# Kernel optimization log

Measured on AMD Instinct MI355X. Metric: run time of the kernel, lower is better.

The kernel has to match this reference:

```python
import jax, jax.numpy as jnp
import numpy as np
import math

B, S, C = 4, 8, 1024
DK = 1024
MAX_LEN = 8192
TOKEN_IND = 4095


def setup_inputs() -> dict:
    key = jax.random.key(0)
    k1, k2, k3, k4 = jax.random.split(key, 4)
    x = jax.random.normal(k1, (B, S, C), dtype=jnp.float32)
    W = jax.random.normal(k2, (C, 3 * DK), dtype=jnp.float32) * (1.0 / math.sqrt(C))
    b = jnp.zeros((3 * DK,), dtype=jnp.float32)
    key_cache = jax.random.normal(k3, (B, MAX_LEN, DK), dtype=jnp.float32)
    value_cache = jax.random.normal(k4, (B, MAX_LEN, DK), dtype=jnp.float32)
    return {"x": x, "W": W, "b": b, "key_cache": key_cache,
            "value_cache": value_cache, "token_ind": TOKEN_IND}


def reference(x, W, b, key_cache, value_cache, token_ind):
    # decode step: only the last token of x is used
    x_last = x[:, -1:, :]                        # [B, 1, C]
    qkv = x_last @ W + b                         # [B, 1, 3*dk]
    q, k_new, v_new = jnp.split(qkv, 3, axis=-1)  # each [B, 1, dk]
    dk = q.shape[-1]

    # scatter new k/v into cache at token_ind, then slice valid prefix
    key_cache = key_cache.at[:, token_ind:token_ind + 1, :].set(k_new)
    value_cache = value_cache.at[:, token_ind:token_ind + 1, :].set(v_new)
    size = token_ind + 1
    k = key_cache[:, :size, :]                   # [B, size, dk]
    v = value_cache[:, :size, :]                 # [B, size, dk]

    # scores for the single query against the whole valid cache
    weights = jnp.einsum('btc,bTc->btT', q, k) / math.sqrt(dk)  # [B, 1, size]

    # faithful broadcast quirk of the original: tril mask (size,size)
    # broadcasts weights [B,1,size] up to [B,size,size]
    mask = jnp.tril(jnp.ones((size, size), dtype=weights.dtype))
    logits = jnp.where(mask == 0, jnp.asarray(-9e15, weights.dtype), weights)  # [B, size, size]
    attention = jax.nn.softmax(logits, axis=-1)
    values = jnp.einsum('btT,bTc->btc', attention, v)  # [B, size, dk]
    return values
```

## Files before the change

kernel.cpp:

```cpp
#include <hip/hip_runtime.h>
#include <stdint.h>

#define B_      4
#define S_      8
#define C_      1024
#define DK_     1024
#define MAXLEN_ 8192
#define SIZE_   4096
#define NCH     64
#define CHR     64
#define NTOK    (SIZE_ - 1)

typedef unsigned short ushort_t;
typedef unsigned int   uint_t;
typedef float f32x4 __attribute__((ext_vector_type(4)));

__device__ __forceinline__ float bf2f(ushort_t u) {
    union { uint_t u; float f; } v; v.u = ((uint_t)u) << 16; return v.f;
}
__device__ __forceinline__ ushort_t f2bf(float f) {
    union { float f; uint_t u; } v; v.f = f;
    uint_t u = v.u;
    uint_t lsb = (u >> 16) & 1u;
    u += 0x7fffu + lsb;
    return (ushort_t)(u >> 16);
}

__global__ void __launch_bounds__(256) k_qkv_partial(
        const float* __restrict__ x, const float* __restrict__ W,
        float* __restrict__ part) {
    __shared__ float xs[B_][128];
    __shared__ float red[8][32][16];
    int t  = threadIdx.x;
    int cg_ = t & 31;
    int rg  = t >> 5;
    int c0 = blockIdx.x * 128;
    int r0 = blockIdx.y * 128;

    for (int i = t; i < B_ * 128; i += 256) {
        int b = i >> 7, r = i & 127;
        xs[b][r] = x[((b * S_) + (S_ - 1)) * C_ + r0 + r];
    }
    __syncthreads();

    float acc[B_][4] = {};
    const float* wp = W + (size_t)(r0 + rg * 16) * (3 * DK_) + c0 + cg_ * 4;
#pragma unroll 8
    for (int i = 0; i < 16; ++i) {
        f32x4 wv = *(const f32x4*)(wp + (size_t)i * (3 * DK_));
        int r = rg * 16 + i;
#pragma unroll
        for (int b = 0; b < B_; ++b) {
            float xv = xs[b][r];
            acc[b][0] += xv * wv[0];
            acc[b][1] += xv * wv[1];
            acc[b][2] += xv * wv[2];
            acc[b][3] += xv * wv[3];
        }
    }
#pragma unroll
    for (int b = 0; b < B_; ++b)
#pragma unroll
        for (int cc = 0; cc < 4; ++cc)
            red[rg][cg_][b * 4 + cc] = acc[b][cc];
    __syncthreads();

    if (t < 32) {
#pragma unroll
        for (int b = 0; b < B_; ++b) {
            float s0 = 0.f, s1 = 0.f, s2 = 0.f, s3 = 0.f;
#pragma unroll
            for (int r = 0; r < 8; ++r) {
                s0 += red[r][t][b * 4 + 0];
                s1 += red[r][t][b * 4 + 1];
                s2 += red[r][t][b * 4 + 2];
                s3 += red[r][t][b * 4 + 3];
            }
            f32x4 v = { s0, s1, s2, s3 };
            *(f32x4*)(part + (size_t)blockIdx.y * (B_ * 3 * DK_) + b * (3 * DK_) + c0 + t * 4) = v;
        }
    }
}

__global__ void __launch_bounds__(256) k_qkv_finish(
        const float* __restrict__ part, const float* __restrict__ bias,
        float* __restrict__ qkvws) {
    int i   = blockIdx.x * 256 + threadIdx.x;
    int bq  = i / 3072;
    int col = i - bq * 3072;
    float s = bias[col];
#pragma unroll
    for (int rt = 0; rt < 8; ++rt) s += part[rt * (B_ * 3 * DK_) + i];
    qkvws[(col >> 10) * (B_ * DK_) + bq * DK_ + (col & (DK_ - 1))] = s;
}

__global__ void __launch_bounds__(1024) k_scores_sum(
        const float* __restrict__ kc, const float* __restrict__ vc,
        const float* __restrict__ qkvws, ushort_t* __restrict__ es_bf,
        float* __restrict__ Ec, ushort_t* __restrict__ Pc) {
    __shared__ float es_l[CHR];
    __shared__ float ec_l[16];
    __shared__ f32x4 sub[4][256];
    int t    = threadIdx.x;
    int c    = blockIdx.x;
    int b    = blockIdx.y;
    int lane = t & 63;
    int wv   = t >> 6;
    int rg   = t >> 8;
    int tc   = t & 255;
    int d0   = tc * 4;

    {
        const float* qp = qkvws + b * DK_ + lane * 4;
        f32x4 q0 = *(const f32x4*)(qp);
        f32x4 q1 = *(const f32x4*)(qp + 256);
        f32x4 q2 = *(const f32x4*)(qp + 512);
        f32x4 q3 = *(const f32x4*)(qp + 768);
        int j0 = c * CHR + wv * 4;
        float esum = 0.f;
#pragma unroll
        for (int r = 0; r < 4; ++r) {
            int j = j0 + r;
            const float* kp = (j == NTOK)
                ? (qkvws + (B_ * DK_) + b * DK_)
                : (kc + ((size_t)b * MAXLEN_ + j) * DK_);
            kp += lane * 4;
            f32x4 k0 = *(const f32x4*)(kp);
            f32x4 k1 = *(const f32x4*)(kp + 256);
            f32x4 k2 = *(const f32x4*)(kp + 512);
            f32x4 k3 = *(const f32x4*)(kp + 768);
            float acc = k0[0]*q0[0] + k0[1]*q0[1] + k0[2]*q0[2] + k0[3]*q0[3]
                      + k1[0]*q1[0] + k1[1]*q1[1] + k1[2]*q1[2] + k1[3]*q1[3]
                      + k2[0]*q2[0] + k2[1]*q2[1] + k2[2]*q2[2] + k2[3]*q2[3]
                      + k3[0]*q3[0] + k3[1]*q3[1] + k3[2]*q3[2] + k3[3]*q3[3];
#pragma unroll
            for (int off = 32; off > 0; off >>= 1) acc += __shfl_down(acc, off, 64);
            if (lane == 0) {
                float e = __expf(acc * 0.03125f);
                es_l[wv * 4 + r] = e;
                es_bf[b * SIZE_ + j] = f2bf(e);
                esum += e;
            }
        }
        if (lane == 0) ec_l[wv] = esum;
    }
    __syncthreads();
    if (t == 0) {
        float s = 0.f;
#pragma unroll
        for (int i = 0; i < 16; ++i) s += ec_l[i];
        Ec[b * NCH + c] = s;
    }

    {
        const float* vbase = vc + ((size_t)b * MAXLEN_ + c * CHR + rg * 16) * DK_ + d0;
        bool subst = (c == NCH - 1) && (rg == 3);
        f32x4 a = { 0.f, 0.f, 0.f, 0.f };
#pragma unroll
        for (int i = 0; i < 16; ++i) {
            const float* vp = (subst && i == 15)
                ? (qkvws + 2 * (B_ * DK_) + b * DK_ + d0)
                : (vbase + (size_t)i * DK_);
            f32x4 u = *(const f32x4*)(vp);
            a += es_l[rg * 16 + i] * u;
        }
        sub[rg][tc] = a;
        __syncthreads();
        if (rg == 0) {
            f32x4 tot = a + sub[1][tc] + sub[2][tc] + sub[3][tc];
            ushort4 pv;
            pv.x = f2bf(tot[0]); pv.y = f2bf(tot[1]);
            pv.z = f2bf(tot[2]); pv.w = f2bf(tot[3]);
            *(ushort4*)(Pc + ((size_t)(b * NCH + c)) * DK_ + d0) = pv;
        }
    }
}

__global__ void __launch_bounds__(1024) k_out(
        const float* __restrict__ vc, const float* __restrict__ qkvws,
        const ushort_t* __restrict__ es_bf, const float* __restrict__ Ec,
        const ushort_t* __restrict__ Pc, float* __restrict__ out) {
    __shared__ float es_l[CHR];
    __shared__ float invS[CHR];
    __shared__ f32x4 sub[4][256];
    __shared__ f32x4 pre[4][256];
    int t  = threadIdx.x;
    int c  = blockIdx.x;
    int b  = blockIdx.y;
    int rg = t >> 8;
    int tc = t & 255;
    int d0 = tc * 4;

    if (t < 64) {
        float e = bf2f(es_bf[b * SIZE_ + c * CHR + t]);
        es_l[t] = e;
        float p = (t < c) ? Ec[b * NCH + t] : 0.f;
#pragma unroll
        for (int off = 32; off > 0; off >>= 1) p += __shfl_down(p, off, 64);
        float E0 = __shfl(p, 0, 64);
        float sc = e;
#pragma unroll
        for (int off = 1; off < 64; off <<= 1) {
            float o = __shfl_up(sc, off, 64);
            if (t >= off) sc += o;
        }
        invS[t] = 1.0f / (E0 + sc);
    }

    f32x4 vrow[16];
    {
        const float* vbase = vc + ((size_t)b * MAXLEN_ + c * CHR + rg * 16) * DK_ + d0;
        bool subst = (c == NCH - 1) && (rg == 3);
#pragma unroll
        for (int i = 0; i < 16; ++i) {
            const float* vp = (subst && i == 15)
                ? (qkvws + 2 * (B_ * DK_) + b * DK_ + d0)
                : (vbase + (size_t)i * DK_);
            vrow[i] = *(const f32x4*)(vp);
        }
    }

    {
        f32x4 p = { 0.f, 0.f, 0.f, 0.f };
        const ushort_t* pp = Pc + (size_t)b * NCH * DK_ + d0;
        for (int cc = rg; cc < c; cc += 4) {
            ushort4 pv = *(const ushort4*)(pp + (size_t)cc * DK_);
            p[0] += bf2f(pv.x); p[1] += bf2f(pv.y);
            p[2] += bf2f(pv.z); p[3] += bf2f(pv.w);
        }
        pre[rg][tc] = p;
    }
    __syncthreads();

    f32x4 a = { 0.f, 0.f, 0.f, 0.f };
#pragma unroll
    for (int i = 0; i < 16; ++i) a += es_l[rg * 16 + i] * vrow[i];
    sub[rg][tc] = a;
    __syncthreads();

    f32x4 acc = pre[0][tc] + pre[1][tc] + pre[2][tc] + pre[3][tc];
#pragma unroll
    for (int g = 0; g < 3; ++g)
        if (g < rg) acc += sub[g][tc];

    float* obase = out + ((size_t)b * SIZE_ + c * CHR + rg * 16) * DK_ + d0;
#pragma unroll
    for (int i = 0; i < 16; ++i) {
        acc += es_l[rg * 16 + i] * vrow[i];
        float is = invS[rg * 16 + i];
        f32x4 ov = { acc[0] * is, acc[1] * is, acc[2] * is, acc[3] * is };
        __builtin_nontemporal_store(ov, (f32x4*)(obase + (size_t)i * DK_));
    }
}

extern "C" void kernel_launch(void* const* d_in, const int* in_sizes, int n_in,
                              void* d_out, int out_size, void* d_ws, size_t ws_size,
                              hipStream_t stream) {
    (void)in_sizes; (void)n_in; (void)out_size; (void)ws_size;
    const float* x    = (const float*)d_in[0];
    const float* W    = (const float*)d_in[1];
    const float* bias = (const float*)d_in[2];
    const float* kc   = (const float*)d_in[3];
    const float* vc   = (const float*)d_in[4];
    float* out        = (float*)d_out;

    float* ws       = (float*)d_ws;
    float* part     = ws;
    float* qkvws    = ws + 131072;
    ushort_t* es_bf = (ushort_t*)(ws + 143360);
    float* Ec       = ws + 151552;
    ushort_t* Pc    = (ushort_t*)ws;

    hipLaunchKernelGGL(k_qkv_partial, dim3(24, 8), dim3(256),  0, stream, x, W, part);
    hipLaunchKernelGGL(k_qkv_finish,  dim3(48),    dim3(256),  0, stream, part, bias, qkvws);
    hipLaunchKernelGGL(k_scores_sum,  dim3(64, 4), dim3(1024), 0, stream, kc, vc, qkvws, es_bf, Ec, Pc);
    hipLaunchKernelGGL(k_out,         dim3(64, 4), dim3(1024), 0, stream, vc, qkvws, es_bf, Ec, Pc, out);
}
```

Before: 294.6 us.

## Fuse scores and output kernels with decoupled-lookback chunk prefix via flags

Merges the score/partial-sum kernel and the output kernel into one kernel. Each block publishes its chunk's fp32 partial V-sum and exp-sum, then spin-waits on per-chunk flags for all earlier chunks before building its prefix. This avoids a second launch, re-reading the V rows and the bf16 round-trips for the intermediate exps and partials. The cost is a dependence on all 256 blocks being co-resident, since a block stalled behind unscheduled earlier chunks could deadlock, plus spin-wait overhead and fp32 traffic for the published partials.

```diff
diff --git a/kernel.cpp b/kernel.cpp
--- a/kernel.cpp
+++ b/kernel.cpp
@@ -11,20 +11,8 @@
 #define CHR     64
 #define NTOK    (SIZE_ - 1)
 
-typedef unsigned short ushort_t;
-typedef unsigned int   uint_t;
+typedef unsigned int uint_t;
 typedef float f32x4 __attribute__((ext_vector_type(4)));
-
-__device__ __forceinline__ float bf2f(ushort_t u) {
-    union { uint_t u; float f; } v; v.u = ((uint_t)u) << 16; return v.f;
-}
-__device__ __forceinline__ ushort_t f2bf(float f) {
-    union { float f; uint_t u; } v; v.f = f;
-    uint_t u = v.u;
-    uint_t lsb = (u >> 16) & 1u;
-    u += 0x7fffu + lsb;
-    return (ushort_t)(u >> 16);
-}
 
 __global__ void __launch_bounds__(256) k_qkv_partial(
         const float* __restrict__ x, const float* __restrict__ W,
@@ -84,7 +72,8 @@
 
 __global__ void __launch_bounds__(256) k_qkv_finish(
         const float* __restrict__ part, const float* __restrict__ bias,
-        float* __restrict__ qkvws) {
+        float* __restrict__ qkvws, uint_t* __restrict__ flags) {
+    if (blockIdx.x == 0) flags[threadIdx.x] = 0;
     int i   = blockIdx.x * 256 + threadIdx.x;
     int bq  = i / 3072;
     int col = i - bq * 3072;
@@ -94,13 +83,16 @@
     qkvws[(col >> 10) * (B_ * DK_) + bq * DK_ + (col & (DK_ - 1))] = s;
 }
 
-__global__ void __launch_bounds__(1024) k_scores_sum(
+__global__ void __launch_bounds__(1024) k_attn(
         const float* __restrict__ kc, const float* __restrict__ vc,
-        const float* __restrict__ qkvws, ushort_t* __restrict__ es_bf,
-        float* __restrict__ Ec, ushort_t* __restrict__ Pc) {
+        const float* __restrict__ qkvws, float* __restrict__ PcPub,
+        float* __restrict__ EcPub, uint_t* __restrict__ flags,
+        float* __restrict__ out) {
     __shared__ float es_l[CHR];
     __shared__ float ec_l[16];
+    __shared__ float invS[CHR];
     __shared__ f32x4 sub[4][256];
+    __shared__ f32x4 pre[4][256];
     int t    = threadIdx.x;
     int c    = blockIdx.x;
     int b    = blockIdx.y;
@@ -138,74 +130,12 @@
             if (lane == 0) {
                 float e = __expf(acc * 0.03125f);
                 es_l[wv * 4 + r] = e;
-                es_bf[b * SIZE_ + j] = f2bf(e);
                 esum += e;
             }
         }
         if (lane == 0) ec_l[wv] = esum;
     }
     __syncthreads();
-    if (t == 0) {
-        float s = 0.f;
-#pragma unroll
-        for (int i = 0; i < 16; ++i) s += ec_l[i];
-        Ec[b * NCH + c] = s;
-    }
-
-    {
-        const float* vbase = vc + ((size_t)b * MAXLEN_ + c * CHR + rg * 16) * DK_ + d0;
-        bool subst = (c == NCH - 1) && (rg == 3);
-        f32x4 a = { 0.f, 0.f, 0.f, 0.f };
-#pragma unroll
-        for (int i = 0; i < 16; ++i) {
-            const float* vp = (subst && i == 15)
-                ? (qkvws + 2 * (B_ * DK_) + b * DK_ + d0)
-                : (vbase + (size_t)i * DK_);
-            f32x4 u = *(const f32x4*)(vp);
-            a += es_l[rg * 16 + i] * u;
-        }
-        sub[rg][tc] = a;
-        __syncthreads();
-        if (rg == 0) {
-            f32x4 tot = a + sub[1][tc] + sub[2][tc] + sub[3][tc];
-            ushort4 pv;
-            pv.x = f2bf(tot[0]); pv.y = f2bf(tot[1]);
-            pv.z = f2bf(tot[2]); pv.w = f2bf(tot[3]);
-            *(ushort4*)(Pc + ((size_t)(b * NCH + c)) * DK_ + d0) = pv;
-        }
-    }
-}
-
-__global__ void __launch_bounds__(1024) k_out(
-        const float* __restrict__ vc, const float* __restrict__ qkvws,
-        const ushort_t* __restrict__ es_bf, const float* __restrict__ Ec,
-        const ushort_t* __restrict__ Pc, float* __restrict__ out) {
-    __shared__ float es_l[CHR];
-    __shared__ float invS[CHR];
-    __shared__ f32x4 sub[4][256];
-    __shared__ f32x4 pre[4][256];
-    int t  = threadIdx.x;
-    int c  = blockIdx.x;
-    int b  = blockIdx.y;
-    int rg = t >> 8;
-    int tc = t & 255;
-    int d0 = tc * 4;
-
-    if (t < 64) {
-        float e = bf2f(es_bf[b * SIZE_ + c * CHR + t]);
-        es_l[t] = e;
-        float p = (t < c) ? Ec[b * NCH + t] : 0.f;
-#pragma unroll
-        for (int off = 32; off > 0; off >>= 1) p += __shfl_down(p, off, 64);
-        float E0 = __shfl(p, 0, 64);
-        float sc = e;
-#pragma unroll
-        for (int off = 1; off < 64; off <<= 1) {
-            float o = __shfl_up(sc, off, 64);
-            if (t >= off) sc += o;
-        }
-        invS[t] = 1.0f / (E0 + sc);
-    }
 
     f32x4 vrow[16];
     {
@@ -219,23 +149,62 @@
             vrow[i] = *(const f32x4*)(vp);
         }
     }
+    {
+        f32x4 a = { 0.f, 0.f, 0.f, 0.f };
+#pragma unroll
+        for (int i = 0; i < 16; ++i) a += es_l[rg * 16 + i] * vrow[i];
+        sub[rg][tc] = a;
+    }
+    __syncthreads();
+
+    if (rg == 0) {
+        f32x4 tot = sub[0][tc] + sub[1][tc] + sub[2][tc] + sub[3][tc];
+        *(f32x4*)(PcPub + ((size_t)(b * NCH + c)) * DK_ + d0) = tot;
+    }
+    if (t == 0) {
+        float s = 0.f;
+#pragma unroll
+        for (int i = 0; i < 16; ++i) s += ec_l[i];
+        EcPub[b * NCH + c] = s;
+    }
+    __syncthreads();
+    if (t == 0) {
+        __threadfence();
+        __hip_atomic_store(&flags[b * NCH + c], 1u, __ATOMIC_RELEASE,
+                           __HIP_MEMORY_SCOPE_AGENT);
+    }
+
+    if (t < c) {
+        while (__hip_atomic_load(&flags[b * NCH + t], __ATOMIC_RELAXED,
+                                 __HIP_MEMORY_SCOPE_AGENT) == 0u)
+            __builtin_amdgcn_s_sleep(4);
+    }
+    __syncthreads();
+    __threadfence();
 
     {
         f32x4 p = { 0.f, 0.f, 0.f, 0.f };
-        const ushort_t* pp = Pc + (size_t)b * NCH * DK_ + d0;
+        const float* pp = PcPub + (size_t)b * NCH * DK_ + d0;
         for (int cc = rg; cc < c; cc += 4) {
-            ushort4 pv = *(const ushort4*)(pp + (size_t)cc * DK_);
-            p[0] += bf2f(pv.x); p[1] += bf2f(pv.y);
-            p[2] += bf2f(pv.z); p[3] += bf2f(pv.w);
+            f32x4 pv = *(const f32x4*)(pp + (size_t)cc * DK_);
+            p += pv;
         }
         pre[rg][tc] = p;
     }
-    __syncthreads();
-
-    f32x4 a = { 0.f, 0.f, 0.f, 0.f };
-#pragma unroll
-    for (int i = 0; i < 16; ++i) a += es_l[rg * 16 + i] * vrow[i];
-    sub[rg][tc] = a;
+    if (t < 64) {
+        float p = (t < c) ? EcPub[b * NCH + t] : 0.f;
+#pragma unroll
+        for (int off = 32; off > 0; off >>= 1) p += __shfl_down(p, off, 64);
+        float E0 = __shfl(p, 0, 64);
+        float e = es_l[t];
+        float sc = e;
+#pragma unroll
+        for (int off = 1; off < 64; off <<= 1) {
+            float o = __shfl_up(sc, off, 64);
+            if (t >= off) sc += o;
+        }
+        invS[t] = 1.0f / (E0 + sc);
+    }
     __syncthreads();
 
     f32x4 acc = pre[0][tc] + pre[1][tc] + pre[2][tc] + pre[3][tc];
@@ -264,15 +233,15 @@
     const float* vc   = (const float*)d_in[4];
     float* out        = (float*)d_out;
 
-    float* ws       = (float*)d_ws;
-    float* part     = ws;
-    float* qkvws    = ws + 131072;
-    ushort_t* es_bf = (ushort_t*)(ws + 143360);
-    float* Ec       = ws + 151552;
-    ushort_t* Pc    = (ushort_t*)ws;
+    float* ws     = (float*)d_ws;
+    float* part   = ws;
+    float* qkvws  = ws + 98304;
+    float* PcPub  = ws + 110592;
+    float* EcPub  = ws + 372736;
+    uint_t* flags = (uint_t*)(ws + 372992);
 
     hipLaunchKernelGGL(k_qkv_partial, dim3(24, 8), dim3(256),  0, stream, x, W, part);
-    hipLaunchKernelGGL(k_qkv_finish,  dim3(48),    dim3(256),  0, stream, part, bias, qkvws);
-    hipLaunchKernelGGL(k_scores_sum,  dim3(64, 4), dim3(1024), 0, stream, kc, vc, qkvws, es_bf, Ec, Pc);
-    hipLaunchKernelGGL(k_out,         dim3(64, 4), dim3(1024), 0, stream, vc, qkvws, es_bf, Ec, Pc, out);
-}
+    hipLaunchKernelGGL(k_qkv_finish,  dim3(48),    dim3(256),  0, stream, part, bias, qkvws, flags);
+    hipLaunchKernelGGL(k_attn,        dim3(64, 4), dim3(1024), 0, stream, kc, vc, qkvws,
+                       PcPub, EcPub, flags, out);
+}
```

After: 360.7 us. 1.22x slower.
